# Performance work log

Hardware: AMD Instinct MI355X
Metric: run time of the kernel (lower is better)

## Reference

```python
import jax, jax.numpy as jnp
import numpy as np

D_MODEL = 1024
NHEAD = 16
HEAD_DIM = D_MODEL // NHEAD
LN_EPS = 1e-5


def setup_inputs() -> dict:
    key = jax.random.key(0)
    ks = jax.random.split(key, 6)
    B, S = 4, 4096
    x = jax.random.normal(ks[0], (B, S, D_MODEL), dtype=jnp.float32)
    scale = 0.02
    Wq = jax.random.normal(ks[1], (D_MODEL, D_MODEL), dtype=jnp.float32) * scale
    Wv = jax.random.normal(ks[2], (D_MODEL, D_MODEL), dtype=jnp.float32) * scale
    Wo = jax.random.normal(ks[3], (D_MODEL, D_MODEL), dtype=jnp.float32) * scale
    Wg = jax.random.normal(ks[4], (D_MODEL, D_MODEL), dtype=jnp.float32) * scale
    beta = jnp.full((NHEAD,), -0.2, dtype=jnp.float32)
    ln_gamma = jnp.ones((D_MODEL,), dtype=jnp.float32)
    ln_beta = jnp.zeros((D_MODEL,), dtype=jnp.float32)
    return {"x": x, "Wq": Wq, "Wv": Wv, "Wo": Wo, "Wg": Wg,
            "beta": beta, "ln_gamma": ln_gamma, "ln_beta": ln_beta}


def _ema_scan(lam, v):
    # v: [B, S, H, D]; lam: [1, 1, H, 1]
    # s_t = lam * s_{t-1} + v_t, computed with a parallel associative scan
    # on pairs (a, b) representing the affine map s -> a*s + b.
    a = jnp.broadcast_to(lam, v.shape)

    def combine(e1, e2):
        a1, b1 = e1
        a2, b2 = e2
        return a1 * a2, a2 * b1 + b2

    _, state = jax.lax.associative_scan(combine, (a, v), axis=1)
    return state


def reference(x, Wq, Wv, Wo, Wg, beta, ln_gamma, ln_beta):
    B, S, _ = x.shape
    q = (x @ Wq.T).reshape(B, S, NHEAD, HEAD_DIM)
    v = (x @ Wv.T).reshape(B, S, NHEAD, HEAD_DIM)
    lam = jax.nn.sigmoid(beta).reshape(1, 1, NHEAD, 1).astype(v.dtype)
    state = _ema_scan(lam, v)                      # [B, S, H, D]
    y = (q * state).reshape(B, S, D_MODEL)
    # LayerNorm over last dim
    mu = jnp.mean(y, axis=-1, keepdims=True)
    var = jnp.mean(jnp.square(y - mu), axis=-1, keepdims=True)
    y = (y - mu) * jax.lax.rsqrt(var + LN_EPS) * ln_gamma + ln_beta
    gate = jax.nn.silu(x @ Wg.T)
    y = y * gate
    return y @ Wo.T
```

## Files before the change

### kernel.cpp

```cpp
#include <hip/hip_runtime.h>

#define D_MODEL 1024
#define NHEAD 16
#define LN_EPS 1e-5f
#define CHUNK 64
#define S_LEN 4096

typedef unsigned short u16;
typedef __attribute__((ext_vector_type(8))) short short8;
typedef __attribute__((ext_vector_type(4))) float f32x4;

__device__ __forceinline__ u16 f2b(float f) {
  unsigned u = __builtin_bit_cast(unsigned, f);
  u += 0x7FFFu + ((u >> 16) & 1u);
  return (u16)(u >> 16);
}
__device__ __forceinline__ float b2f(u16 s) {
  return __builtin_bit_cast(float, ((unsigned)s) << 16);
}

__global__ __launch_bounds__(256) void cvt_f32_bf16(const float4* __restrict__ src,
                                                    ushort4* __restrict__ dst, int n4) {
  int i = blockIdx.x * blockDim.x + threadIdx.x;
  int stride = gridDim.x * blockDim.x;
  for (; i < n4; i += stride) {
    float4 f = src[i];
    ushort4 o;
    o.x = f2b(f.x); o.y = f2b(f.y); o.z = f2b(f.z); o.w = f2b(f.w);
    dst[i] = o;
  }
}

__global__ void lam_kernel(const float* __restrict__ beta, float* __restrict__ lam) {
  int h = threadIdx.x;
  if (h < NHEAD) lam[h] = 1.f / (1.f + __expf(-beta[h]));
}


#define SLOT (256 * 32)

__device__ __forceinline__ void glds16(const u16* g, const u16* l) {
  __builtin_amdgcn_global_load_lds(
      (const __attribute__((address_space(1))) unsigned*)g,
      (__attribute__((address_space(3))) unsigned*)l, 16, 0, 0);
}

template <typename OutT>
__global__ __launch_bounds__(512, 2) void gemm256(const u16* __restrict__ X,
                                                  const u16* __restrict__ W,
                                                  OutT* __restrict__ Out,
                                                  int M, int N, int K) {
  __shared__ u16 sm[3][2][SLOT];
  const int tid = threadIdx.x;
  const int lane = tid & 63;
  const int wave = tid >> 6;
  const int ln15 = lane & 15, lh = lane >> 4;
  const int wr = wave >> 2, wc = wave & 3;
  const int bm = blockIdx.x * 256, bn = blockIdx.y * 256;
  const int NT = K >> 5;

  const int lrow = lane >> 2;
  const int lcol = (lane & 3) << 3;

  const u16* Ag = X + (size_t)(bm + wave * 32 + lrow) * K + lcol;
  const u16* Bg = W + (size_t)(bn + wave * 32 + lrow) * K + lcol;
  const int lw = wave * 1024;

  const int aoff = (wr * 128 + ln15) * 32 + lh * 8;
  const int boff = (wc * 64 + ln15) * 32 + lh * 8;

  f32x4 acc[8][4];
  f32x4 zero = {0.f, 0.f, 0.f, 0.f};
  #pragma unroll
  for (int m = 0; m < 8; ++m)
    #pragma unroll
    for (int n = 0; n < 4; ++n) acc[m][n] = zero;

  #pragma unroll
  for (int tt = 0; tt < 2; ++tt) {
    const u16* Agt = Ag + tt * 32;
    const u16* Bgt = Bg + tt * 32;
    glds16(Agt,          sm[tt][0] + lw);
    glds16(Agt + 16 * K, sm[tt][0] + lw + 512);
    glds16(Bgt,          sm[tt][1] + lw);
    glds16(Bgt + 16 * K, sm[tt][1] + lw + 512);
  }
  asm volatile("s_waitcnt vmcnt(4)" ::: "memory");
  asm volatile("s_barrier" ::: "memory");

  for (int t = 0; t < NT; ++t) {
    const int cur = t % 3;
    const int nb = (t + 2) % 3;
    const int t2 = t + 2;
    const bool st = (t2 < NT);
    const u16* fA = sm[cur][0] + aoff;
    const u16* fB = sm[cur][1] + boff;
    const u16* Agt = Ag + t2 * 32;
    const u16* Bgt = Bg + t2 * 32;

    short8 a[8], b[4];
    #pragma unroll
    for (int m = 0; m < 4; ++m) a[m] = *(const short8*)(fA + m * 512);
    b[0] = *(const short8*)(fB);
    b[1] = *(const short8*)(fB + 512);
    if (st) glds16(Agt, sm[nb][0] + lw);
    asm volatile("s_barrier" ::: "memory");
    __builtin_amdgcn_sched_barrier(0);
    __builtin_amdgcn_s_setprio(1);
    #pragma unroll
    for (int m = 0; m < 4; ++m)
      #pragma unroll
      for (int n = 0; n < 2; ++n)
        acc[m][n] = __builtin_amdgcn_mfma_f32_16x16x32_bf16(a[m], b[n], acc[m][n], 0, 0, 0);
    __builtin_amdgcn_s_setprio(0);
    __builtin_amdgcn_sched_barrier(0);
    asm volatile("s_barrier" ::: "memory");

    #pragma unroll
    for (int m = 4; m < 8; ++m) a[m] = *(const short8*)(fA + m * 512);
    b[2] = *(const short8*)(fB + 2 * 512);
    b[3] = *(const short8*)(fB + 3 * 512);
    if (st) glds16(Agt + 16 * K, sm[nb][0] + lw + 512);
    asm volatile("s_barrier" ::: "memory");
    __builtin_amdgcn_sched_barrier(0);
    __builtin_amdgcn_s_setprio(1);
    #pragma unroll
    for (int m = 4; m < 8; ++m)
      #pragma unroll
      for (int n = 0; n < 2; ++n)
        acc[m][n] = __builtin_amdgcn_mfma_f32_16x16x32_bf16(a[m], b[n], acc[m][n], 0, 0, 0);
    __builtin_amdgcn_s_setprio(0);
    __builtin_amdgcn_sched_barrier(0);
    asm volatile("s_barrier" ::: "memory");

    if (st) glds16(Bgt, sm[nb][1] + lw);
    __builtin_amdgcn_sched_barrier(0);
    __builtin_amdgcn_s_setprio(1);
    #pragma unroll
    for (int m = 0; m < 4; ++m)
      #pragma unroll
      for (int n = 2; n < 4; ++n)
        acc[m][n] = __builtin_amdgcn_mfma_f32_16x16x32_bf16(a[m], b[n], acc[m][n], 0, 0, 0);
    __builtin_amdgcn_s_setprio(0);
    __builtin_amdgcn_sched_barrier(0);
    asm volatile("s_barrier" ::: "memory");

    if (st) glds16(Bgt + 16 * K, sm[nb][1] + lw + 512);
    __builtin_amdgcn_sched_barrier(0);
    __builtin_amdgcn_s_setprio(1);
    #pragma unroll
    for (int m = 4; m < 8; ++m)
      #pragma unroll
      for (int n = 2; n < 4; ++n)
        acc[m][n] = __builtin_amdgcn_mfma_f32_16x16x32_bf16(a[m], b[n], acc[m][n], 0, 0, 0);
    __builtin_amdgcn_s_setprio(0);
    __builtin_amdgcn_sched_barrier(0);
    if (t < NT - 2) {
      asm volatile("s_waitcnt vmcnt(4)" ::: "memory");
    } else if (t == NT - 2) {
      asm volatile("s_waitcnt vmcnt(0)" ::: "memory");
    }
    asm volatile("s_barrier" ::: "memory");
  }

  #pragma unroll
  for (int m = 0; m < 8; ++m)
    #pragma unroll
    for (int n = 0; n < 4; ++n)
      #pragma unroll
      for (int r = 0; r < 4; ++r) {
        int row = bm + wr * 128 + m * 16 + lh * 4 + r;
        int col = bn + wc * 64 + n * 16 + ln15;
        float vv = acc[m][n][r];
        if constexpr (sizeof(OutT) == 2) Out[(size_t)row * N + col] = f2b(vv);
        else                             Out[(size_t)row * N + col] = vv;
      }
}

__global__ __launch_bounds__(256) void scan_local(u16* __restrict__ v,
                                                  float* __restrict__ carry,
                                                  const float* __restrict__ lam,
                                                  int S, int nch, int ld) {
  int bj = blockIdx.x;
  int b = bj / nch, j = bj - b * nch;
  int col0 = threadIdx.x * 4;
  float l = lam[col0 >> 6];
  float s0 = 0.f, s1 = 0.f, s2 = 0.f, s3 = 0.f;
  size_t base = ((size_t)b * S + (size_t)j * CHUNK) * ld + col0;
  for (int t = 0; t < CHUNK; ++t) {
    ushort4* p = (ushort4*)(v + base + (size_t)t * ld);
    ushort4 u = *p;
    s0 = l * s0 + b2f(u.x);
    s1 = l * s1 + b2f(u.y);
    s2 = l * s2 + b2f(u.z);
    s3 = l * s3 + b2f(u.w);
    u.x = f2b(s0); u.y = f2b(s1); u.z = f2b(s2); u.w = f2b(s3);
    *p = u;
  }
  size_t cb = (size_t)bj * D_MODEL + col0;
  carry[cb] = s0; carry[cb + 1] = s1; carry[cb + 2] = s2; carry[cb + 3] = s3;
}

__global__ void scan_carry(float* __restrict__ carry, const float* __restrict__ lam,
                           int B, int nch) {
  int idx = blockIdx.x * blockDim.x + threadIdx.x;
  if (idx >= B * D_MODEL) return;
  int b = idx >> 10, col = idx & (D_MODEL - 1);
  float l = lam[col >> 6];
  float lC = __powf(l, (float)CHUNK);
  float c = 0.f;
  for (int j = 0; j < nch; ++j) {
    size_t a = ((size_t)(b * nch + j)) * D_MODEL + col;
    c = lC * c + carry[a];
    carry[a] = c;
  }
}

__global__ __launch_bounds__(256) void ew_ln(const u16* __restrict__ qvg,
    const float* __restrict__ carry, const float* __restrict__ lam,
    const float* __restrict__ gamma, const float* __restrict__ lbeta,
    u16* __restrict__ yout, int S, int nch, int ld) {
  int row = blockIdx.x;
  int b = row / S, s = row - b * S;
  int j = s / CHUNK, tl = s - j * CHUNK;
  int tid = threadIdx.x;
  int col0 = tid * 4;
  size_t rb = (size_t)row * ld;

  ushort4 qu = *(const ushort4*)(qvg + rb + col0);
  ushort4 su = *(const ushort4*)(qvg + rb + D_MODEL + col0);
  float st[4] = {b2f(su.x), b2f(su.y), b2f(su.z), b2f(su.w)};
  if (j > 0) {
    float l = lam[col0 >> 6];
    float p = __powf(l, (float)(tl + 1));
    const float4 c4 = *(const float4*)(carry + ((size_t)(b * nch + j - 1)) * D_MODEL + col0);
    st[0] += p * c4.x; st[1] += p * c4.y; st[2] += p * c4.z; st[3] += p * c4.w;
  }
  float q[4] = {b2f(qu.x), b2f(qu.y), b2f(qu.z), b2f(qu.w)};
  float y[4];
  float sum = 0.f, sumsq = 0.f;
  #pragma unroll
  for (int i = 0; i < 4; ++i) {
    y[i] = q[i] * st[i];
    sum += y[i];
    sumsq += y[i] * y[i];
  }
  #pragma unroll
  for (int off = 32; off > 0; off >>= 1) {
    sum += __shfl_down(sum, off);
    sumsq += __shfl_down(sumsq, off);
  }
  __shared__ float red[8];
  int ln = tid & 63, wv = tid >> 6;
  if (ln == 0) { red[wv] = sum; red[4 + wv] = sumsq; }
  __syncthreads();
  sum = red[0] + red[1] + red[2] + red[3];
  sumsq = red[4] + red[5] + red[6] + red[7];
  float mu = sum * (1.f / 1024.f);
  float var = sumsq * (1.f / 1024.f) - mu * mu;
  float rstd = rsqrtf(var + LN_EPS);

  float4 gm = *(const float4*)(gamma + col0);
  float4 bt = *(const float4*)(lbeta + col0);
  ushort4 gu = *(const ushort4*)(qvg + rb + 2 * D_MODEL + col0);
  float gv[4]  = {b2f(gu.x), b2f(gu.y), b2f(gu.z), b2f(gu.w)};
  float gmv[4] = {gm.x, gm.y, gm.z, gm.w};
  float btv[4] = {bt.x, bt.y, bt.z, bt.w};
  u16 ov[4];
  #pragma unroll
  for (int i = 0; i < 4; ++i) {
    float gate = gv[i] / (1.f + __expf(-gv[i]));
    float oo = ((y[i] - mu) * rstd * gmv[i] + btv[i]) * gate;
    ov[i] = f2b(oo);
  }
  ushort4 o; o.x = ov[0]; o.y = ov[1]; o.z = ov[2]; o.w = ov[3];
  *(ushort4*)(yout + (size_t)row * D_MODEL + col0) = o;
}

extern "C" void kernel_launch(void* const* d_in, const int* in_sizes, int n_in,
                              void* d_out, int out_size, void* d_ws, size_t ws_size,
                              hipStream_t stream) {
  const float* x     = (const float*)d_in[0];
  const float* Wq    = (const float*)d_in[1];
  const float* Wv    = (const float*)d_in[2];
  const float* Wo    = (const float*)d_in[3];
  const float* Wg    = (const float*)d_in[4];
  const float* beta  = (const float*)d_in[5];
  const float* gamma = (const float*)d_in[6];
  const float* lbeta = (const float*)d_in[7];
  float* out = (float*)d_out;

  const int BS = in_sizes[0] / D_MODEL;
  const int S = S_LEN;
  const int B = BS / S;
  const int nch = S / CHUNK;
  const size_t nx = (size_t)BS * D_MODEL;
  const size_t nw = (size_t)D_MODEL * D_MODEL;
  const int N3 = 3 * D_MODEL;

  char* w = (char*)d_ws;
  u16* xb   = (u16*)w;  w += nx * 2;
  u16* wqvg = (u16*)w;  w += 3 * nw * 2;
  u16* wob  = (u16*)w;  w += nw * 2;
  u16* qvg  = (u16*)w;  w += (size_t)BS * N3 * 2;
  u16* yb   = (u16*)w;  w += nx * 2;
  float* carry = (float*)w;  w += (size_t)B * nch * D_MODEL * 4;
  float* lam = (float*)w;

  cvt_f32_bf16<<<2048, 256, 0, stream>>>((const float4*)x,  (ushort4*)xb, (int)(nx / 4));
  cvt_f32_bf16<<<1024, 256, 0, stream>>>((const float4*)Wq, (ushort4*)(wqvg), (int)(nw / 4));
  cvt_f32_bf16<<<1024, 256, 0, stream>>>((const float4*)Wv, (ushort4*)(wqvg + nw), (int)(nw / 4));
  cvt_f32_bf16<<<1024, 256, 0, stream>>>((const float4*)Wg, (ushort4*)(wqvg + 2 * nw), (int)(nw / 4));
  cvt_f32_bf16<<<1024, 256, 0, stream>>>((const float4*)Wo, (ushort4*)wob, (int)(nw / 4));
  lam_kernel<<<1, 64, 0, stream>>>(beta, lam);

  dim3 g1(BS / 256, N3 / 256);
  gemm256<u16><<<g1, 512, 0, stream>>>(xb, wqvg, qvg, BS, N3, D_MODEL);

  scan_local<<<B * nch, 256, 0, stream>>>(qvg + D_MODEL, carry, lam, S, nch, N3);
  scan_carry<<<(B * D_MODEL + 255) / 256, 256, 0, stream>>>(carry, lam, B, nch);
  ew_ln<<<BS, 256, 0, stream>>>(qvg, carry, lam, gamma, lbeta, yb, S, nch, N3);

  dim3 g2(BS / 256, D_MODEL / 256);
  gemm256<float><<<g2, 512, 0, stream>>>(yb, wob, out, BS, D_MODEL, D_MODEL);
}
```

Measured before the change: 276.6 us.

## Rework GEMM main loop to K=64 tiles with XOR-swizzled LDS and split-buffer staging

The bf16 GEMM now processes K in 64-wide tiles instead of 32, halving the number of loop iterations and barriers per K step. The LDS tiles are stored with an XOR swizzle on 16-byte columns to cut bank conflicts on fragment reads. Loads are staged per half-tile into eight 16KB buffers, with B prefetched one tile ahead and A two tiles ahead. The buffer footprint and register pressure grow, since each wave now holds twice the fragments, which may affect the two-blocks-per-CU occupancy target.

```diff
diff --git a/kernel.cpp b/kernel.cpp
--- a/kernel.cpp
+++ b/kernel.cpp
@@ -37,37 +37,44 @@
 }
 
 
-#define SLOT (256 * 32)
-
 __device__ __forceinline__ void glds16(const u16* g, const u16* l) {
   __builtin_amdgcn_global_load_lds(
       (const __attribute__((address_space(1))) unsigned*)g,
       (__attribute__((address_space(3))) unsigned*)l, 16, 0, 0);
 }
+
+#define BAR() asm volatile("s_barrier" ::: "memory")
 
 template <typename OutT>
 __global__ __launch_bounds__(512, 2) void gemm256(const u16* __restrict__ X,
                                                   const u16* __restrict__ W,
                                                   OutT* __restrict__ Out,
                                                   int M, int N, int K) {
-  __shared__ u16 sm[3][2][SLOT];
+  __shared__ u16 sm[8][8192];
   const int tid = threadIdx.x;
   const int lane = tid & 63;
   const int wave = tid >> 6;
   const int ln15 = lane & 15, lh = lane >> 4;
   const int wr = wave >> 2, wc = wave & 3;
   const int bm = blockIdx.x * 256, bn = blockIdx.y * 256;
-  const int NT = K >> 5;
-
-  const int lrow = lane >> 2;
-  const int lcol = (lane & 3) << 3;
-
-  const u16* Ag = X + (size_t)(bm + wave * 32 + lrow) * K + lcol;
-  const u16* Bg = W + (size_t)(bn + wave * 32 + lrow) * K + lcol;
-  const int lw = wave * 1024;
-
-  const int aoff = (wr * 128 + ln15) * 32 + lh * 8;
-  const int boff = (wc * 64 + ln15) * 32 + lh * 8;
+  const int NT = K >> 6;
+
+  const int srow = tid >> 3;
+  const int scol = ((tid & 7) ^ (srow & 7)) << 3;
+  const u16* Asrc = X + (size_t)(bm + srow) * K + scol;
+  const u16* Bsrc = W + (size_t)(bn + srow) * K + scol;
+  const int ldsw = wave * 512;
+
+#define STAGE(u, h, tile, src)                                          \
+  { const u16* _g = (src) + (size_t)((h) * 128) * K + (tile) * 64;      \
+    glds16(_g,                 &sm[u][ldsw]);                           \
+    glds16(_g + (size_t)64 * K, &sm[u][ldsw + 4096]); }
+
+  const char* smb = (const char*)&sm[0][0];
+  const char* Ard = smb + wr * 16384 + ln15 * 128;
+  const char* Brd = smb + (2 + (wc >> 1)) * 16384 + ((wc & 1) * 64 + ln15) * 128;
+  const int swz0 = ((lh ^ (ln15 & 7)) << 4);
+  const int swz1 = (((4 + lh) ^ (ln15 & 7)) << 4);
 
   f32x4 acc[8][4];
   f32x4 zero = {0.f, 0.f, 0.f, 0.f};
@@ -76,92 +83,107 @@
     #pragma unroll
     for (int n = 0; n < 4; ++n) acc[m][n] = zero;
 
-  #pragma unroll
-  for (int tt = 0; tt < 2; ++tt) {
-    const u16* Agt = Ag + tt * 32;
-    const u16* Bgt = Bg + tt * 32;
-    glds16(Agt,          sm[tt][0] + lw);
-    glds16(Agt + 16 * K, sm[tt][0] + lw + 512);
-    glds16(Bgt,          sm[tt][1] + lw);
-    glds16(Bgt + 16 * K, sm[tt][1] + lw + 512);
-  }
+  STAGE(0, 0, 0, Asrc); STAGE(1, 1, 0, Asrc);
+  STAGE(2, 0, 0, Bsrc); STAGE(3, 1, 0, Bsrc);
+  STAGE(4, 0, 1, Asrc); STAGE(5, 1, 1, Asrc);
   asm volatile("s_waitcnt vmcnt(4)" ::: "memory");
-  asm volatile("s_barrier" ::: "memory");
+  BAR();
 
   for (int t = 0; t < NT; ++t) {
-    const int cur = t % 3;
-    const int nb = (t + 2) % 3;
-    const int t2 = t + 2;
-    const bool st = (t2 < NT);
-    const u16* fA = sm[cur][0] + aoff;
-    const u16* fB = sm[cur][1] + boff;
-    const u16* Agt = Ag + t2 * 32;
-    const u16* Bgt = Bg + t2 * 32;
-
-    short8 a[8], b[4];
-    #pragma unroll
-    for (int m = 0; m < 4; ++m) a[m] = *(const short8*)(fA + m * 512);
-    b[0] = *(const short8*)(fB);
-    b[1] = *(const short8*)(fB + 512);
-    if (st) glds16(Agt, sm[nb][0] + lw);
-    asm volatile("s_barrier" ::: "memory");
+    const int d = t & 1;
+    const int db = d * 65536;
+    const int od = (d ^ 1) * 4;
+    const int sd = d * 4;
+    short8 a[8][2], b[4][2];
+
+    #pragma unroll
+    for (int m = 0; m < 4; ++m) {
+      a[m][0] = *(const short8*)(Ard + db + m * 2048 + swz0);
+      a[m][1] = *(const short8*)(Ard + db + m * 2048 + swz1);
+    }
+    #pragma unroll
+    for (int n = 0; n < 2; ++n) {
+      b[n][0] = *(const short8*)(Brd + db + n * 2048 + swz0);
+      b[n][1] = *(const short8*)(Brd + db + n * 2048 + swz1);
+    }
+    if (t + 1 < NT) STAGE(od + 2, 0, t + 1, Bsrc);
+    BAR();
+    asm volatile("s_waitcnt lgkmcnt(0)" ::: "memory");
     __builtin_amdgcn_sched_barrier(0);
     __builtin_amdgcn_s_setprio(1);
     #pragma unroll
     for (int m = 0; m < 4; ++m)
       #pragma unroll
-      for (int n = 0; n < 2; ++n)
-        acc[m][n] = __builtin_amdgcn_mfma_f32_16x16x32_bf16(a[m], b[n], acc[m][n], 0, 0, 0);
+      for (int n = 0; n < 2; ++n) {
+        acc[m][n] = __builtin_amdgcn_mfma_f32_16x16x32_bf16(a[m][0], b[n][0], acc[m][n], 0, 0, 0);
+        acc[m][n] = __builtin_amdgcn_mfma_f32_16x16x32_bf16(a[m][1], b[n][1], acc[m][n], 0, 0, 0);
+      }
     __builtin_amdgcn_s_setprio(0);
     __builtin_amdgcn_sched_barrier(0);
-    asm volatile("s_barrier" ::: "memory");
-
-    #pragma unroll
-    for (int m = 4; m < 8; ++m) a[m] = *(const short8*)(fA + m * 512);
-    b[2] = *(const short8*)(fB + 2 * 512);
-    b[3] = *(const short8*)(fB + 3 * 512);
-    if (st) glds16(Agt + 16 * K, sm[nb][0] + lw + 512);
-    asm volatile("s_barrier" ::: "memory");
+    BAR();
+
+    #pragma unroll
+    for (int m = 4; m < 8; ++m) {
+      a[m][0] = *(const short8*)(Ard + db + m * 2048 + swz0);
+      a[m][1] = *(const short8*)(Ard + db + m * 2048 + swz1);
+    }
+    if (t + 1 < NT) STAGE(od + 3, 1, t + 1, Bsrc);
+    BAR();
+    asm volatile("s_waitcnt lgkmcnt(0)" ::: "memory");
     __builtin_amdgcn_sched_barrier(0);
     __builtin_amdgcn_s_setprio(1);
     #pragma unroll
     for (int m = 4; m < 8; ++m)
       #pragma unroll
-      for (int n = 0; n < 2; ++n)
-        acc[m][n] = __builtin_amdgcn_mfma_f32_16x16x32_bf16(a[m], b[n], acc[m][n], 0, 0, 0);
+      for (int n = 0; n < 2; ++n) {
+        acc[m][n] = __builtin_amdgcn_mfma_f32_16x16x32_bf16(a[m][0], b[n][0], acc[m][n], 0, 0, 0);
+        acc[m][n] = __builtin_amdgcn_mfma_f32_16x16x32_bf16(a[m][1], b[n][1], acc[m][n], 0, 0, 0);
+      }
     __builtin_amdgcn_s_setprio(0);
     __builtin_amdgcn_sched_barrier(0);
-    asm volatile("s_barrier" ::: "memory");
-
-    if (st) glds16(Bgt, sm[nb][1] + lw);
+    BAR();
+
+    #pragma unroll
+    for (int n = 2; n < 4; ++n) {
+      b[n][0] = *(const short8*)(Brd + db + n * 2048 + swz0);
+      b[n][1] = *(const short8*)(Brd + db + n * 2048 + swz1);
+    }
+    if (t + 2 < NT) STAGE(sd + 0, 0, t + 2, Asrc);
+    BAR();
+    asm volatile("s_waitcnt lgkmcnt(0)" ::: "memory");
     __builtin_amdgcn_sched_barrier(0);
     __builtin_amdgcn_s_setprio(1);
     #pragma unroll
     for (int m = 0; m < 4; ++m)
       #pragma unroll
-      for (int n = 2; n < 4; ++n)
-        acc[m][n] = __builtin_amdgcn_mfma_f32_16x16x32_bf16(a[m], b[n], acc[m][n], 0, 0, 0);
+      for (int n = 2; n < 4; ++n) {
+        acc[m][n] = __builtin_amdgcn_mfma_f32_16x16x32_bf16(a[m][0], b[n][0], acc[m][n], 0, 0, 0);
+        acc[m][n] = __builtin_amdgcn_mfma_f32_16x16x32_bf16(a[m][1], b[n][1], acc[m][n], 0, 0, 0);
+      }
     __builtin_amdgcn_s_setprio(0);
     __builtin_amdgcn_sched_barrier(0);
-    asm volatile("s_barrier" ::: "memory");
-
-    if (st) glds16(Bgt + 16 * K, sm[nb][1] + lw + 512);
+    BAR();
+
+    if (t + 2 < NT) STAGE(sd + 1, 1, t + 2, Asrc);
     __builtin_amdgcn_sched_barrier(0);
     __builtin_amdgcn_s_setprio(1);
     #pragma unroll
     for (int m = 4; m < 8; ++m)
       #pragma unroll
-      for (int n = 2; n < 4; ++n)
-        acc[m][n] = __builtin_amdgcn_mfma_f32_16x16x32_bf16(a[m], b[n], acc[m][n], 0, 0, 0);
+      for (int n = 2; n < 4; ++n) {
+        acc[m][n] = __builtin_amdgcn_mfma_f32_16x16x32_bf16(a[m][0], b[n][0], acc[m][n], 0, 0, 0);
+        acc[m][n] = __builtin_amdgcn_mfma_f32_16x16x32_bf16(a[m][1], b[n][1], acc[m][n], 0, 0, 0);
+      }
     __builtin_amdgcn_s_setprio(0);
     __builtin_amdgcn_sched_barrier(0);
-    if (t < NT - 2) {
+    if (t + 2 < NT) {
       asm volatile("s_waitcnt vmcnt(4)" ::: "memory");
-    } else if (t == NT - 2) {
+    } else if (t + 1 < NT) {
       asm volatile("s_waitcnt vmcnt(0)" ::: "memory");
     }
-    asm volatile("s_barrier" ::: "memory");
-  }
+    BAR();
+  }
+#undef STAGE
 
   #pragma unroll
   for (int m = 0; m < 8; ++m)
```

Measured after the change: 259.2 us. 1.07x faster.
